# Optimization experiments

Hardware: AMD Instinct MI355X
Metric: run time of the kernel (lower is better)

Reference implementation:

```python
import jax, jax.numpy as jnp
import numpy as np

N_NODES = 100_000
N_EDGES = 1_600_000
NUM_GRAPHS = 16_384
F_IN = 4      # PLAYER_FEATURES
HID = 32      # HIDDEN_DIM


def setup_inputs() -> dict:
    key = jax.random.key(0)
    ks = jax.random.split(key, 12)
    x = jax.random.normal(ks[0], (N_NODES, F_IN), jnp.float32)
    edge_index = jax.random.randint(ks[1], (2, N_EDGES), 0, N_NODES, dtype=jnp.int32)
    edge_weight = jax.random.uniform(ks[2], (N_EDGES,), jnp.float32)
    batch = jnp.sort(jax.random.randint(ks[3], (N_NODES,), 0, NUM_GRAPHS, dtype=jnp.int32))
    # GCNConv weights (glorot-ish scale) and biases
    W1 = jax.random.normal(ks[4], (F_IN, HID), jnp.float32) / np.sqrt(F_IN)
    b1 = jnp.zeros((HID,), jnp.float32)
    W2 = jax.random.normal(ks[5], (HID, HID), jnp.float32) / np.sqrt(HID)
    b2 = jnp.zeros((HID,), jnp.float32)
    Wo = jax.random.normal(ks[6], (HID, 1), jnp.float32) / np.sqrt(HID)
    bo = jnp.zeros((1,), jnp.float32)
    Wb = jax.random.normal(ks[7], (HID, 1), jnp.float32) / np.sqrt(HID)
    bb = jnp.zeros((1,), jnp.float32)
    return {"x": x, "edge_index": edge_index, "edge_weight": edge_weight,
            "batch": batch, "num_graphs": NUM_GRAPHS,
            "W1": W1, "b1": b1, "W2": W2, "b2": b2,
            "Wo": Wo, "bo": bo, "Wb": Wb, "bb": bb}


def _gcn_conv(x, src, dst, w, W, b, n):
    # PyG GCNConv: symmetric normalization with self-loops already in (src,dst,w)
    deg = jax.ops.segment_sum(w, dst, num_segments=n)                 # weighted degree [n]
    dinv = jnp.where(deg > 0, jax.lax.rsqrt(deg), 0.0)
    norm = dinv[src] * w * dinv[dst]                                  # [E+n]
    h = x @ W                                                         # transform first
    agg = jax.ops.segment_sum(h[src] * norm[:, None], dst, num_segments=n)
    return agg + b


def reference(x, edge_index, edge_weight, batch, num_graphs,
              W1, b1, W2, b2, Wo, bo, Wb, bb):
    n = x.shape[0]
    loop = jnp.arange(n, dtype=edge_index.dtype)
    src = jnp.concatenate([edge_index[0], loop])   # add self-loops (fill weight 1)
    dst = jnp.concatenate([edge_index[1], loop])
    w = jnp.concatenate([edge_weight, jnp.ones((n,), edge_weight.dtype)])

    h = jax.nn.relu(_gcn_conv(x, src, dst, w, W1, b1, n))
    h = jax.nn.relu(_gcn_conv(h, src, dst, w, W2, b2, n))

    # global_mean_pool over batch assignment
    sums = jax.ops.segment_sum(h, batch, num_segments=num_graphs)
    cnt = jax.ops.segment_sum(jnp.ones((n,), h.dtype), batch, num_segments=num_graphs)
    pooled = sums / jnp.maximum(cnt, 1.0)[:, None]                    # [G, HID]

    orange = jax.nn.sigmoid(pooled @ Wo + bo)                          # [G, 1]
    blue = jax.nn.sigmoid(pooled @ Wb + bb)                            # [G, 1]
    return (orange, blue)
```

## Files before the change

kernel.cpp:

```cpp
#include <hip/hip_runtime.h>
#include <math.h>

#define FIN 4
#define HID 32
#define EPB 4096
#define BUCK_SH 9
#define BUCK_W 512
#define NBUCK_MAX 256
#define CAP 12288

__device__ __forceinline__ unsigned pack_bf16x2(float a, float b) {
    unsigned ua = __float_as_uint(a); ua += 0x7FFF + ((ua >> 16) & 1);
    unsigned ub = __float_as_uint(b); ub += 0x7FFF + ((ub >> 16) & 1);
    return (ua >> 16) | (ub & 0xFFFF0000u);
}
__device__ __forceinline__ float bf_lo(unsigned u) { return __uint_as_float(u << 16); }
__device__ __forceinline__ float bf_hi(unsigned u) { return __uint_as_float(u & 0xFFFF0000u); }
__device__ __forceinline__ float dec_w(unsigned u) { return ((float)(u >> 17) + 0.5f) * (1.0f / 32768.0f); }

__global__ void p1a_bounds(const int* __restrict__ dst, const int* __restrict__ batch,
                           int* __restrict__ counts, int* __restrict__ gstart,
                           int E, int n, int nbuck, int G) {
    __shared__ int h[4][NBUCK_MAX];
    int t = threadIdx.x;
    int wv = t >> 6;
    for (int q = t; q < 4 * NBUCK_MAX; q += 256) ((int*)h)[q] = 0;
    __syncthreads();
    int base = blockIdx.x * EPB;
    for (int k = t; k < EPB; k += 256) {
        int e = base + k;
        if (e < E) atomicAdd(&h[wv][dst[e] >> BUCK_SH], 1);
    }
    __syncthreads();
    for (int q = t; q < nbuck; q += 256)
        counts[blockIdx.x * nbuck + q] = h[0][q] + h[1][q] + h[2][q] + h[3][q];
    int i = blockIdx.x * 256 + t;
    if (i < n) {
        int b = batch[i];
        if (i == 0) {
            for (int g = 0; g <= b; ++g) gstart[g] = 0;
        } else {
            int p = batch[i - 1];
            for (int g = p + 1; g <= b; ++g) gstart[g] = i;
        }
        if (i == n - 1) {
            for (int g = b + 1; g <= G; ++g) gstart[g] = n;
        }
    }
}

__global__ void rowscan_kernel(const int* __restrict__ counts, int* __restrict__ offsets,
                               int* __restrict__ bucketCnt, int nblk, int nbuck) {
    __shared__ int s[512];
    int b = blockIdx.x;
    int t = threadIdx.x;
    int v = (t < nblk) ? counts[t * nbuck + b] : 0;
    s[t] = v;
    __syncthreads();
    for (int off = 1; off < 512; off <<= 1) {
        int u = (t >= off) ? s[t - off] : 0;
        __syncthreads();
        s[t] += u;
        __syncthreads();
    }
    if (t < nblk) offsets[t * nbuck + b] = b * CAP + s[t] - v;
    if (t == nblk - 1) bucketCnt[b] = s[t];
}

__global__ void p1c_scatter(const int* __restrict__ src, const int* __restrict__ dst,
                            const float* __restrict__ w, const int* __restrict__ offsets,
                            unsigned long long* __restrict__ bkt, int E, int nbuck) {
    __shared__ int cur[NBUCK_MAX];
    int t = threadIdx.x;
    for (int q = t; q < nbuck; q += 256) cur[q] = offsets[blockIdx.x * nbuck + q];
    __syncthreads();
    int base = blockIdx.x * EPB;
    for (int k = t; k < EPB; k += 256) {
        int e = base + k;
        if (e < E) {
            int d = dst[e];
            int sN = src[e];
            float wv = w[e];
            unsigned wfix = (unsigned)(wv * 32768.0f);
            wfix = wfix > 32767u ? 32767u : wfix;
            int b = d >> BUCK_SH;
            int pos = atomicAdd(&cur[b], 1);
            unsigned hi = ((unsigned)(d & (BUCK_W - 1)) << 17) | (unsigned)sN;
            bkt[pos] = ((unsigned long long)hi << 32) | wfix;
        }
    }
}

__global__ __launch_bounds__(1024) void p2_csr(
        const unsigned long long* __restrict__ bkt, const int* __restrict__ bucketCnt,
        const float* __restrict__ x, unsigned* __restrict__ csr4,
        int* __restrict__ rowptr, int* __restrict__ cntv,
        float* __restrict__ dinv, float* __restrict__ xs, int n) {
    __shared__ int lcnt[BUCK_W];
    __shared__ int s[BUCK_W];
    __shared__ int curL[BUCK_W];
    __shared__ int wsumI[BUCK_W];
    int b = blockIdx.x;
    int t = threadIdx.x;
    int base = b * CAP;
    int cnt  = bucketCnt[b];
    if (t < BUCK_W) { lcnt[t] = 0; wsumI[t] = 0; }
    __syncthreads();
    for (int k = t; k < cnt; k += 1024) {
        unsigned long long v = bkt[base + k];
        unsigned hi = (unsigned)(v >> 32);
        atomicAdd(&lcnt[hi >> 17], 1);
        atomicAdd(&wsumI[hi >> 17], (int)(unsigned)v);
    }
    __syncthreads();
    if (t < BUCK_W) s[t] = lcnt[t];
    __syncthreads();
    for (int off = 1; off < BUCK_W; off <<= 1) {
        int v = (t < BUCK_W && t >= off) ? s[t - off] : 0;
        __syncthreads();
        if (t < BUCK_W) s[t] += v;
        __syncthreads();
    }
    int node = (b << BUCK_SH) + t;
    if (t < BUCK_W) {
        int excl = s[t] - lcnt[t];
        curL[t] = excl;
        if (node < n) { rowptr[node] = base + excl; cntv[node] = lcnt[t]; }
    }
    __syncthreads();
    for (int k = t; k < cnt; k += 1024) {
        unsigned long long v = bkt[base + k];
        unsigned hi = (unsigned)(v >> 32);
        unsigned wfix = (unsigned)v;
        int ld = hi >> 17;
        int sN = hi & 0x1FFFF;
        int p = atomicAdd(&curL[ld], 1);
        csr4[base + p] = (wfix << 17) | (unsigned)sN;
    }
    __syncthreads();
    if (t < BUCK_W && node < n) {
        float wsum = ((float)wsumI[t] + 0.5f * (float)lcnt[t]) * (1.0f / 32768.0f);
        float di = rsqrtf(wsum + 1.0f);
        dinv[node] = di;
        float4 xv = *reinterpret_cast<const float4*>(x + (size_t)node * FIN);
        xv.x *= di; xv.y *= di; xv.z *= di; xv.w *= di;
        *reinterpret_cast<float4*>(xs + (size_t)node * FIN) = xv;
    }
}

__global__ void layer1_kernel(const float* __restrict__ xs, const int* __restrict__ rowptr,
                              const int* __restrict__ cntv, const unsigned* __restrict__ csr4,
                              const float* __restrict__ dinv, const float* __restrict__ W1,
                              const float* __restrict__ b1, unsigned* __restrict__ h1, int n) {
    __shared__ float sW[FIN * HID];
    __shared__ float sb[HID];
    int t = threadIdx.x;
    if (t < FIN * HID) sW[t] = W1[t];
    if (t < HID) sb[t] = b1[t];
    __syncthreads();
    int i = blockIdx.x * blockDim.x + t;
    if (i >= n) return;
    float di = dinv[i];
    float4 a = *reinterpret_cast<const float4*>(xs + (size_t)i * FIN);
    int beg = rowptr[i], c = cntv[i];
    int j = 0;
    for (; j + 7 < c; j += 8) {
        unsigned u[8];
        float4 v[8];
        #pragma unroll
        for (int q = 0; q < 8; ++q) u[q] = __builtin_nontemporal_load(csr4 + beg + j + q);
        #pragma unroll
        for (int q = 0; q < 8; ++q) v[q] = *reinterpret_cast<const float4*>(xs + (size_t)(u[q] & 0x1FFFF) * FIN);
        #pragma unroll
        for (int q = 0; q < 8; ++q) {
            float wq = dec_w(u[q]);
            a.x += wq * v[q].x; a.y += wq * v[q].y; a.z += wq * v[q].z; a.w += wq * v[q].w;
        }
    }
    for (; j + 3 < c; j += 4) {
        unsigned u[4];
        float4 v[4];
        #pragma unroll
        for (int q = 0; q < 4; ++q) u[q] = __builtin_nontemporal_load(csr4 + beg + j + q);
        #pragma unroll
        for (int q = 0; q < 4; ++q) v[q] = *reinterpret_cast<const float4*>(xs + (size_t)(u[q] & 0x1FFFF) * FIN);
        #pragma unroll
        for (int q = 0; q < 4; ++q) {
            float wq = dec_w(u[q]);
            a.x += wq * v[q].x; a.y += wq * v[q].y; a.z += wq * v[q].z; a.w += wq * v[q].w;
        }
    }
    for (; j < c; ++j) {
        unsigned u0 = __builtin_nontemporal_load(csr4 + beg + j);
        float w0 = dec_w(u0);
        float4 v0 = *reinterpret_cast<const float4*>(xs + (size_t)(u0 & 0x1FFFF) * FIN);
        a.x += w0*v0.x; a.y += w0*v0.y; a.z += w0*v0.z; a.w += w0*v0.w;
    }
    a.x *= di; a.y *= di; a.z *= di; a.w *= di;
    unsigned pk[16];
    #pragma unroll
    for (int k = 0; k < HID; k += 2) {
        float h0 = fmaxf(sb[k]   + a.x*sW[0*HID+k]   + a.y*sW[1*HID+k]   + a.z*sW[2*HID+k]   + a.w*sW[3*HID+k],   0.f);
        float h1v= fmaxf(sb[k+1] + a.x*sW[0*HID+k+1] + a.y*sW[1*HID+k+1] + a.z*sW[2*HID+k+1] + a.w*sW[3*HID+k+1], 0.f);
        pk[k / 2] = pack_bf16x2(di * h0, di * h1v);
    }
    uint4* hp = reinterpret_cast<uint4*>(h1 + (size_t)i * 16);
    hp[0] = make_uint4(pk[0], pk[1], pk[2], pk[3]);
    hp[1] = make_uint4(pk[4], pk[5], pk[6], pk[7]);
    hp[2] = make_uint4(pk[8], pk[9], pk[10], pk[11]);
    hp[3] = make_uint4(pk[12], pk[13], pk[14], pk[15]);
}

__global__ __launch_bounds__(256) void layer2_kernel(
        const unsigned* __restrict__ h1, const int* __restrict__ rowptr,
        const int* __restrict__ cntv, const unsigned* __restrict__ csr4,
        const float* __restrict__ dinv, const float* __restrict__ W2,
        const float* __restrict__ b2, unsigned* __restrict__ h2, int n) {
    __shared__ float sW[HID * HID];
    __shared__ float sb[HID];
    __shared__ float sAgg[32][HID + 1];
    int t = threadIdx.x;
    for (int q = t; q < HID * HID; q += 256) sW[q] = W2[q];
    if (t < HID) sb[t] = b2[t];
    __syncthreads();
    int nib = t >> 3;
    int l   = t & 7;
    int i = blockIdx.x * 32 + nib;
    const uint2* h1d = reinterpret_cast<const uint2*>(h1);
    float a0, a1, a2, a3;
    if (i < n) {
        uint2 hv = h1d[(size_t)i * 8 + l];
        a0 = bf_lo(hv.x);
        a1 = bf_hi(hv.x);
        a2 = bf_lo(hv.y);
        a3 = bf_hi(hv.y);
        int beg = rowptr[i], c = cntv[i];
        int j = 0;
        for (; j + 7 < c; j += 8) {
            unsigned u[8];
            uint2 sv[8];
            #pragma unroll
            for (int q = 0; q < 8; ++q) u[q] = __builtin_nontemporal_load(csr4 + beg + j + q);
            #pragma unroll
            for (int q = 0; q < 8; ++q) sv[q] = h1d[(size_t)(u[q] & 0x1FFFF) * 8 + l];
            #pragma unroll
            for (int q = 0; q < 8; ++q) {
                float wq = dec_w(u[q]);
                a0 += wq * bf_lo(sv[q].x);
                a1 += wq * bf_hi(sv[q].x);
                a2 += wq * bf_lo(sv[q].y);
                a3 += wq * bf_hi(sv[q].y);
            }
        }
        for (; j + 3 < c; j += 4) {
            unsigned u[4];
            uint2 sv[4];
            #pragma unroll
            for (int q = 0; q < 4; ++q) u[q] = __builtin_nontemporal_load(csr4 + beg + j + q);
            #pragma unroll
            for (int q = 0; q < 4; ++q) sv[q] = h1d[(size_t)(u[q] & 0x1FFFF) * 8 + l];
            #pragma unroll
            for (int q = 0; q < 4; ++q) {
                float wq = dec_w(u[q]);
                a0 += wq * bf_lo(sv[q].x);
                a1 += wq * bf_hi(sv[q].x);
                a2 += wq * bf_lo(sv[q].y);
                a3 += wq * bf_hi(sv[q].y);
            }
        }
        for (; j < c; ++j) {
            unsigned u0 = __builtin_nontemporal_load(csr4 + beg + j);
            float w0 = dec_w(u0);
            uint2 s0 = h1d[(size_t)(u0 & 0x1FFFF) * 8 + l];
            a0 += w0 * bf_lo(s0.x);
            a1 += w0 * bf_hi(s0.x);
            a2 += w0 * bf_lo(s0.y);
            a3 += w0 * bf_hi(s0.y);
        }
        float di = dinv[i];
        a0 *= di; a1 *= di; a2 *= di; a3 *= di;
    } else {
        a0 = a1 = a2 = a3 = 0.f;
    }
    sAgg[nib][l * 4 + 0] = a0;
    sAgg[nib][l * 4 + 1] = a1;
    sAgg[nib][l * 4 + 2] = a2;
    sAgg[nib][l * 4 + 3] = a3;
    __syncthreads();
    if (i < n) {
        int k0 = l * 4;
        float o0 = sb[k0], o1 = sb[k0 + 1], o2 = sb[k0 + 2], o3 = sb[k0 + 3];
        #pragma unroll
        for (int j2 = 0; j2 < HID; ++j2) {
            float av = sAgg[nib][j2];
            o0 += av * sW[j2 * HID + k0];
            o1 += av * sW[j2 * HID + k0 + 1];
            o2 += av * sW[j2 * HID + k0 + 2];
            o3 += av * sW[j2 * HID + k0 + 3];
        }
        uint2 pkd;
        pkd.x = pack_bf16x2(fmaxf(o0, 0.f), fmaxf(o1, 0.f));
        pkd.y = pack_bf16x2(fmaxf(o2, 0.f), fmaxf(o3, 0.f));
        reinterpret_cast<uint2*>(h2)[(size_t)i * 8 + l] = pkd;
    }
}

__global__ void poolheads_kernel(const unsigned* __restrict__ h2, const int* __restrict__ gstart,
                                 const float* __restrict__ Wo, const float* __restrict__ bo,
                                 const float* __restrict__ Wb, const float* __restrict__ bb,
                                 float* __restrict__ out, int G) {
    int g = blockIdx.x * 4 + (threadIdx.x >> 6);
    int lane = threadIdx.x & 63;
    int k = lane & 31;
    int half = lane >> 5;
    if (g >= G) return;
    int s0 = gstart[g], s1 = gstart[g + 1];
    float sum = 0.f;
    const unsigned short* h2s = reinterpret_cast<const unsigned short*>(h2);
    for (int i = s0 + half; i < s1; i += 2) {
        unsigned u = (unsigned)h2s[(size_t)i * HID + k] << 16;
        sum += __uint_as_float(u);
    }
    float cnt = (float)(s1 - s0);
    float inv = 1.0f / fmaxf(cnt, 1.0f);
    float m = sum * inv;
    float po = m * Wo[k];
    float pb = m * Wb[k];
    #pragma unroll
    for (int off = 32; off >= 1; off >>= 1) {
        po += __shfl_xor(po, off);
        pb += __shfl_xor(pb, off);
    }
    if (lane == 0) {
        out[g]     = 1.0f / (1.0f + expf(-(po + bo[0])));
        out[G + g] = 1.0f / (1.0f + expf(-(pb + bb[0])));
    }
}

extern "C" void kernel_launch(void* const* d_in, const int* in_sizes, int n_in,
                              void* d_out, int out_size, void* d_ws, size_t ws_size,
                              hipStream_t stream) {
    const float* x     = (const float*)d_in[0];
    const int*   ei    = (const int*)d_in[1];
    const float* ew    = (const float*)d_in[2];
    const int*   batch = (const int*)d_in[3];
    const float* W1 = (const float*)d_in[5];
    const float* b1 = (const float*)d_in[6];
    const float* W2 = (const float*)d_in[7];
    const float* b2 = (const float*)d_in[8];
    const float* Wo = (const float*)d_in[9];
    const float* bo = (const float*)d_in[10];
    const float* Wb = (const float*)d_in[11];
    const float* bb = (const float*)d_in[12];
    float* out = (float*)d_out;

    const int n = in_sizes[0] / FIN;
    const int E = in_sizes[2];
    const int G = out_size / 2;
    const int* src = ei;
    const int* dst = ei + E;
    const int n4 = (n + 3) & ~3;
    const int nblk  = (E + EPB - 1) / EPB;
    const int nbuck = (n + BUCK_W - 1) / BUCK_W;
    const int M  = nblk * nbuck;
    const int Mp = (M + 3) & ~3;

    char* wsb = (char*)d_ws;
    unsigned long long* bkt = (unsigned long long*)wsb;
    unsigned* csr4     = (unsigned*)(wsb + (size_t)nbuck * CAP * 8);
    int*      counts   = (int*)(csr4 + (size_t)nbuck * CAP);
    int*      offsets  = counts + Mp;
    int*      bucketCnt= offsets + Mp;
    int*      rowptr   = bucketCnt + 256;
    int*      cntv     = rowptr + n4;
    float*    dinv     = (float*)(cntv + n4);
    float*    xs       = dinv + n4;
    int*      gstart   = (int*)(xs + (size_t)n4 * FIN);
    unsigned* h1       = (unsigned*)(gstart + G + 16);
    unsigned* h2       = h1 + (size_t)n4 * 16;

    const int B = 256;
    p1a_bounds   <<<nblk, 256, 0, stream>>>(dst, batch, counts, gstart, E, n, nbuck, G);
    rowscan_kernel<<<nbuck, 512, 0, stream>>>(counts, offsets, bucketCnt, nblk, nbuck);
    p1c_scatter  <<<nblk, 256, 0, stream>>>(src, dst, ew, offsets, bkt, E, nbuck);
    p2_csr       <<<nbuck, 1024, 0, stream>>>(bkt, bucketCnt, x, csr4, rowptr, cntv, dinv, xs, n);
    layer1_kernel<<<(n + B - 1) / B, B, 0, stream>>>(xs, rowptr, cntv, csr4, dinv, W1, b1, h1, n);
    layer2_kernel<<<(n + 31) / 32, B, 0, stream>>>(h1, rowptr, cntv, csr4, dinv, W2, b2, h2, n);
    poolheads_kernel<<<(G + 3) / 4, B, 0, stream>>>(h2, gstart, Wo, bo, Wb, bb, out, G);
}
```

Measured before the change: 105.4 us.

## Fuse edge bucketing into one pass with global atomic offsets; widen layer2 per-node lanes

The separate histogram, row-scan and scatter kernels become one kernel. It stages edges in shared memory, reserves per-bucket ranges with global atomics on a memset counter array, then scatters from shared memory. This drops one full re-read of the edge arrays and two launches, but makes the bucket order nondeterministic. Layer2 now uses 16 lanes per node, each gathering one packed bf16 pair, to raise gather parallelism. The 4-wide remainder loops are removed.

Measured after the change: 121.7 us. 15.5% more time.

```diff
diff --git a/kernel.cpp b/kernel.cpp
--- a/kernel.cpp
+++ b/kernel.cpp
@@ -18,22 +18,48 @@
 __device__ __forceinline__ float bf_hi(unsigned u) { return __uint_as_float(u & 0xFFFF0000u); }
 __device__ __forceinline__ float dec_w(unsigned u) { return ((float)(u >> 17) + 0.5f) * (1.0f / 32768.0f); }
 
-__global__ void p1a_bounds(const int* __restrict__ dst, const int* __restrict__ batch,
-                           int* __restrict__ counts, int* __restrict__ gstart,
-                           int E, int n, int nbuck, int G) {
-    __shared__ int h[4][NBUCK_MAX];
+__global__ __launch_bounds__(256) void p1c_fused(
+        const int* __restrict__ src, const int* __restrict__ dst,
+        const float* __restrict__ w, const int* __restrict__ batch,
+        int* __restrict__ gcur, unsigned long long* __restrict__ bkt,
+        int* __restrict__ gstart, int E, int n, int nbuck, int G) {
+    __shared__ unsigned hiA[EPB];
+    __shared__ unsigned short wfA[EPB];
+    __shared__ unsigned char bidA[EPB];
+    __shared__ int h[NBUCK_MAX];
+    __shared__ int cur[NBUCK_MAX];
     int t = threadIdx.x;
-    int wv = t >> 6;
-    for (int q = t; q < 4 * NBUCK_MAX; q += 256) ((int*)h)[q] = 0;
+    for (int q = t; q < nbuck; q += 256) h[q] = 0;
     __syncthreads();
     int base = blockIdx.x * EPB;
     for (int k = t; k < EPB; k += 256) {
         int e = base + k;
-        if (e < E) atomicAdd(&h[wv][dst[e] >> BUCK_SH], 1);
+        if (e < E) {
+            int d  = __builtin_nontemporal_load(dst + e);
+            int sN = __builtin_nontemporal_load(src + e);
+            float wv = __builtin_nontemporal_load(w + e);
+            unsigned wfix = (unsigned)(wv * 32768.0f);
+            wfix = wfix > 32767u ? 32767u : wfix;
+            int b = d >> BUCK_SH;
+            hiA[k]  = ((unsigned)(d & (BUCK_W - 1)) << 17) | (unsigned)sN;
+            wfA[k]  = (unsigned short)wfix;
+            bidA[k] = (unsigned char)b;
+            atomicAdd(&h[b], 1);
+        } else {
+            bidA[k] = 0xFF;
+        }
     }
     __syncthreads();
     for (int q = t; q < nbuck; q += 256)
-        counts[blockIdx.x * nbuck + q] = h[0][q] + h[1][q] + h[2][q] + h[3][q];
+        cur[q] = q * CAP + atomicAdd(&gcur[q], h[q]);
+    __syncthreads();
+    for (int k = t; k < EPB; k += 256) {
+        unsigned b = bidA[k];
+        if (b != 0xFF) {
+            int pos = atomicAdd(&cur[b], 1);
+            bkt[pos] = ((unsigned long long)hiA[k] << 32) | wfA[k];
+        }
+    }
     int i = blockIdx.x * 256 + t;
     if (i < n) {
         int b = batch[i];
@@ -45,48 +71,6 @@
         }
         if (i == n - 1) {
             for (int g = b + 1; g <= G; ++g) gstart[g] = n;
-        }
-    }
-}
-
-__global__ void rowscan_kernel(const int* __restrict__ counts, int* __restrict__ offsets,
-                               int* __restrict__ bucketCnt, int nblk, int nbuck) {
-    __shared__ int s[512];
-    int b = blockIdx.x;
-    int t = threadIdx.x;
-    int v = (t < nblk) ? counts[t * nbuck + b] : 0;
-    s[t] = v;
-    __syncthreads();
-    for (int off = 1; off < 512; off <<= 1) {
-        int u = (t >= off) ? s[t - off] : 0;
-        __syncthreads();
-        s[t] += u;
-        __syncthreads();
-    }
-    if (t < nblk) offsets[t * nbuck + b] = b * CAP + s[t] - v;
-    if (t == nblk - 1) bucketCnt[b] = s[t];
-}
-
-__global__ void p1c_scatter(const int* __restrict__ src, const int* __restrict__ dst,
-                            const float* __restrict__ w, const int* __restrict__ offsets,
-                            unsigned long long* __restrict__ bkt, int E, int nbuck) {
-    __shared__ int cur[NBUCK_MAX];
-    int t = threadIdx.x;
-    for (int q = t; q < nbuck; q += 256) cur[q] = offsets[blockIdx.x * nbuck + q];
-    __syncthreads();
-    int base = blockIdx.x * EPB;
-    for (int k = t; k < EPB; k += 256) {
-        int e = base + k;
-        if (e < E) {
-            int d = dst[e];
-            int sN = src[e];
-            float wv = w[e];
-            unsigned wfix = (unsigned)(wv * 32768.0f);
-            wfix = wfix > 32767u ? 32767u : wfix;
-            int b = d >> BUCK_SH;
-            int pos = atomicAdd(&cur[b], 1);
-            unsigned hi = ((unsigned)(d & (BUCK_W - 1)) << 17) | (unsigned)sN;
-            bkt[pos] = ((unsigned long long)hi << 32) | wfix;
         }
     }
 }
@@ -177,19 +161,6 @@
             a.x += wq * v[q].x; a.y += wq * v[q].y; a.z += wq * v[q].z; a.w += wq * v[q].w;
         }
     }
-    for (; j + 3 < c; j += 4) {
-        unsigned u[4];
-        float4 v[4];
-        #pragma unroll
-        for (int q = 0; q < 4; ++q) u[q] = __builtin_nontemporal_load(csr4 + beg + j + q);
-        #pragma unroll
-        for (int q = 0; q < 4; ++q) v[q] = *reinterpret_cast<const float4*>(xs + (size_t)(u[q] & 0x1FFFF) * FIN);
-        #pragma unroll
-        for (int q = 0; q < 4; ++q) {
-            float wq = dec_w(u[q]);
-            a.x += wq * v[q].x; a.y += wq * v[q].y; a.z += wq * v[q].z; a.w += wq * v[q].w;
-        }
-    }
     for (; j < c; ++j) {
         unsigned u0 = __builtin_nontemporal_load(csr4 + beg + j);
         float w0 = dec_w(u0);
@@ -218,90 +189,60 @@
         const float* __restrict__ b2, unsigned* __restrict__ h2, int n) {
     __shared__ float sW[HID * HID];
     __shared__ float sb[HID];
-    __shared__ float sAgg[32][HID + 1];
+    __shared__ float sAgg[16][HID + 1];
     int t = threadIdx.x;
     for (int q = t; q < HID * HID; q += 256) sW[q] = W2[q];
     if (t < HID) sb[t] = b2[t];
     __syncthreads();
-    int nib = t >> 3;
-    int l   = t & 7;
-    int i = blockIdx.x * 32 + nib;
-    const uint2* h1d = reinterpret_cast<const uint2*>(h1);
-    float a0, a1, a2, a3;
+    int nib = t >> 4;
+    int l   = t & 15;
+    int i = blockIdx.x * 16 + nib;
+    float a0, a1;
     if (i < n) {
-        uint2 hv = h1d[(size_t)i * 8 + l];
-        a0 = bf_lo(hv.x);
-        a1 = bf_hi(hv.x);
-        a2 = bf_lo(hv.y);
-        a3 = bf_hi(hv.y);
+        unsigned hv = h1[(size_t)i * 16 + l];
+        a0 = bf_lo(hv);
+        a1 = bf_hi(hv);
         int beg = rowptr[i], c = cntv[i];
         int j = 0;
         for (; j + 7 < c; j += 8) {
             unsigned u[8];
-            uint2 sv[8];
+            unsigned sv[8];
             #pragma unroll
             for (int q = 0; q < 8; ++q) u[q] = __builtin_nontemporal_load(csr4 + beg + j + q);
             #pragma unroll
-            for (int q = 0; q < 8; ++q) sv[q] = h1d[(size_t)(u[q] & 0x1FFFF) * 8 + l];
+            for (int q = 0; q < 8; ++q) sv[q] = h1[(size_t)(u[q] & 0x1FFFF) * 16 + l];
             #pragma unroll
             for (int q = 0; q < 8; ++q) {
                 float wq = dec_w(u[q]);
-                a0 += wq * bf_lo(sv[q].x);
-                a1 += wq * bf_hi(sv[q].x);
-                a2 += wq * bf_lo(sv[q].y);
-                a3 += wq * bf_hi(sv[q].y);
-            }
-        }
-        for (; j + 3 < c; j += 4) {
-            unsigned u[4];
-            uint2 sv[4];
-            #pragma unroll
-            for (int q = 0; q < 4; ++q) u[q] = __builtin_nontemporal_load(csr4 + beg + j + q);
-            #pragma unroll
-            for (int q = 0; q < 4; ++q) sv[q] = h1d[(size_t)(u[q] & 0x1FFFF) * 8 + l];
-            #pragma unroll
-            for (int q = 0; q < 4; ++q) {
-                float wq = dec_w(u[q]);
-                a0 += wq * bf_lo(sv[q].x);
-                a1 += wq * bf_hi(sv[q].x);
-                a2 += wq * bf_lo(sv[q].y);
-                a3 += wq * bf_hi(sv[q].y);
+                a0 += wq * bf_lo(sv[q]);
+                a1 += wq * bf_hi(sv[q]);
             }
         }
         for (; j < c; ++j) {
             unsigned u0 = __builtin_nontemporal_load(csr4 + beg + j);
             float w0 = dec_w(u0);
-            uint2 s0 = h1d[(size_t)(u0 & 0x1FFFF) * 8 + l];
-            a0 += w0 * bf_lo(s0.x);
-            a1 += w0 * bf_hi(s0.x);
-            a2 += w0 * bf_lo(s0.y);
-            a3 += w0 * bf_hi(s0.y);
+            unsigned s0 = h1[(size_t)(u0 & 0x1FFFF) * 16 + l];
+            a0 += w0 * bf_lo(s0);
+            a1 += w0 * bf_hi(s0);
         }
         float di = dinv[i];
-        a0 *= di; a1 *= di; a2 *= di; a3 *= di;
+        a0 *= di; a1 *= di;
     } else {
-        a0 = a1 = a2 = a3 = 0.f;
-    }
-    sAgg[nib][l * 4 + 0] = a0;
-    sAgg[nib][l * 4 + 1] = a1;
-    sAgg[nib][l * 4 + 2] = a2;
-    sAgg[nib][l * 4 + 3] = a3;
+        a0 = a1 = 0.f;
+    }
+    sAgg[nib][l * 2]     = a0;
+    sAgg[nib][l * 2 + 1] = a1;
     __syncthreads();
     if (i < n) {
-        int k0 = l * 4;
-        float o0 = sb[k0], o1 = sb[k0 + 1], o2 = sb[k0 + 2], o3 = sb[k0 + 3];
+        int k0 = l * 2;
+        float o0 = sb[k0], o1 = sb[k0 + 1];
         #pragma unroll
         for (int j2 = 0; j2 < HID; ++j2) {
             float av = sAgg[nib][j2];
             o0 += av * sW[j2 * HID + k0];
             o1 += av * sW[j2 * HID + k0 + 1];
-            o2 += av * sW[j2 * HID + k0 + 2];
-            o3 += av * sW[j2 * HID + k0 + 3];
-        }
-        uint2 pkd;
-        pkd.x = pack_bf16x2(fmaxf(o0, 0.f), fmaxf(o1, 0.f));
-        pkd.y = pack_bf16x2(fmaxf(o2, 0.f), fmaxf(o3, 0.f));
-        reinterpret_cast<uint2*>(h2)[(size_t)i * 8 + l] = pkd;
+        }
+        h2[(size_t)i * 16 + l] = pack_bf16x2(fmaxf(o0, 0.f), fmaxf(o1, 0.f));
     }
 }
 
@@ -362,16 +303,12 @@
     const int n4 = (n + 3) & ~3;
     const int nblk  = (E + EPB - 1) / EPB;
     const int nbuck = (n + BUCK_W - 1) / BUCK_W;
-    const int M  = nblk * nbuck;
-    const int Mp = (M + 3) & ~3;
 
     char* wsb = (char*)d_ws;
     unsigned long long* bkt = (unsigned long long*)wsb;
     unsigned* csr4     = (unsigned*)(wsb + (size_t)nbuck * CAP * 8);
-    int*      counts   = (int*)(csr4 + (size_t)nbuck * CAP);
-    int*      offsets  = counts + Mp;
-    int*      bucketCnt= offsets + Mp;
-    int*      rowptr   = bucketCnt + 256;
+    int*      gcur     = (int*)(csr4 + (size_t)nbuck * CAP);
+    int*      rowptr   = gcur + 256;
     int*      cntv     = rowptr + n4;
     float*    dinv     = (float*)(cntv + n4);
     float*    xs       = dinv + n4;
@@ -380,11 +317,10 @@
     unsigned* h2       = h1 + (size_t)n4 * 16;
 
     const int B = 256;
-    p1a_bounds   <<<nblk, 256, 0, stream>>>(dst, batch, counts, gstart, E, n, nbuck, G);
-    rowscan_kernel<<<nbuck, 512, 0, stream>>>(counts, offsets, bucketCnt, nblk, nbuck);
-    p1c_scatter  <<<nblk, 256, 0, stream>>>(src, dst, ew, offsets, bkt, E, nbuck);
-    p2_csr       <<<nbuck, 1024, 0, stream>>>(bkt, bucketCnt, x, csr4, rowptr, cntv, dinv, xs, n);
+    hipMemsetAsync(gcur, 0, 256 * sizeof(int), stream);
+    p1c_fused    <<<nblk, 256, 0, stream>>>(src, dst, ew, batch, gcur, bkt, gstart, E, n, nbuck, G);
+    p2_csr       <<<nbuck, 1024, 0, stream>>>(bkt, gcur, x, csr4, rowptr, cntv, dinv, xs, n);
     layer1_kernel<<<(n + B - 1) / B, B, 0, stream>>>(xs, rowptr, cntv, csr4, dinv, W1, b1, h1, n);
-    layer2_kernel<<<(n + 31) / 32, B, 0, stream>>>(h1, rowptr, cntv, csr4, dinv, W2, b2, h2, n);
+    layer2_kernel<<<(n + 15) / 16, B, 0, stream>>>(h1, rowptr, cntv, csr4, dinv, W2, b2, h2, n);
     poolheads_kernel<<<(G + 3) / 4, B, 0, stream>>>(h2, gstart, Wo, bo, Wb, bb, out, G);
 }
```
